# Optimization experiments

Measured on AMD Instinct MI355X. Metric: run time of the kernel, lower is better.

The kernel has to match this reference:

```python
import jax, jax.numpy as jnp
import numpy as np

B, H, S, D = 4, 16, 2048, 64

def setup_inputs() -> dict:
    key = jax.random.key(0)
    kq, kk, kv = jax.random.split(key, 3)
    Q = jax.random.normal(kq, (B, H, S, D), dtype=jnp.float32)
    K = jax.random.normal(kk, (B, H, S, D), dtype=jnp.float32)
    V = jax.random.normal(kv, (B, H, S, D), dtype=jnp.float32)
    return {"Q": Q, "K": K, "V": V}

def reference(Q, K, V):
    d_model = Q.shape[-1]
    # [B,H,S,S] scores matrix, materialized as in the original (unfused SDPA)
    scores = jnp.einsum('bhqd,bhkd->bhqk', Q, K) / jnp.sqrt(jnp.float32(d_model))
    attention = jax.nn.softmax(scores, axis=-1)
    out = jnp.einsum('bhqk,bhkd->bhqd', attention, V)
    return out
```

## Files before the change

kernel.cpp:

```cpp
#include <hip/hip_runtime.h>
#include <hip/hip_bf16.h>

namespace {

constexpr int kSeq = 2048;
constexpr int kD   = 64;
constexpr int kBH  = 64;
constexpr int kBM  = 64;
constexpr int kBN  = 64;
constexpr int kNT  = kSeq / kBN;
constexpr int kPs  = 72;

typedef __attribute__((ext_vector_type(8))) short bf16x8;
typedef __attribute__((ext_vector_type(4))) float f32x4;
typedef __attribute__((ext_vector_type(2))) unsigned int u32x2;

__device__ __forceinline__ unsigned short f2bf(float f) {
  unsigned int u = __builtin_bit_cast(unsigned int, f);
  u += 0x7fffu + ((u >> 16) & 1u);
  return (unsigned short)(u >> 16);
}

__device__ __forceinline__ unsigned int pkbf(float a, float b) {
#if __has_builtin(__builtin_amdgcn_cvt_pk_bf16_f32)
  typedef __attribute__((ext_vector_type(2))) __bf16 bfv2;
  bfv2 r = __builtin_amdgcn_cvt_pk_bf16_f32(a, b);
  return __builtin_bit_cast(unsigned int, r);
#else
  unsigned int ua = __builtin_bit_cast(unsigned int, a) + 0x8000u;
  unsigned int ub = __builtin_bit_cast(unsigned int, b) + 0x8000u;
  return __builtin_amdgcn_perm(ub, ua, 0x07060302);
#endif
}

__device__ __forceinline__ float fexp2(float x) {
#if __has_builtin(__builtin_amdgcn_exp2f)
  return __builtin_amdgcn_exp2f(x);
#else
  return exp2f(x);
#endif
}

__device__ __forceinline__ void load16(const unsigned short* g, unsigned short* l) {
  __builtin_amdgcn_global_load_lds(
      (const __attribute__((address_space(1))) unsigned int*)g,
      (__attribute__((address_space(3))) unsigned int*)l, 16, 0, 0);
}

__global__ __launch_bounds__(256) void prep(
    const float* __restrict__ K, const float* __restrict__ V,
    unsigned short* __restrict__ Kbf, unsigned short* __restrict__ Vt) {
  __shared__ unsigned short sT[kD * 72];
  const int tid = threadIdx.x;
  const int bh = blockIdx.x >> 5;
  const int t0 = (blockIdx.x & 31) * 64;
  const float* Kb = K + ((size_t)bh * kSeq + t0) * kD;
  const float* Vb = V + ((size_t)bh * kSeq + t0) * kD;
  unsigned short* Ko = Kbf + ((size_t)bh * kSeq + t0) * kD;
#pragma unroll
  for (int t = 0; t < 4; ++t) {
    const int idx = tid + t * 256;
    const int row = idx >> 4;
    const int c4  = (idx & 15) * 4;
    const float4 k4 = *(const float4*)(Kb + row * kD + c4);
    u32x2 kp = {pkbf(k4.x, k4.y), pkbf(k4.z, k4.w)};
    *(u32x2*)(Ko + row * kD + c4) = kp;
    const float4 v4 = *(const float4*)(Vb + row * kD + c4);
    sT[(c4 + 0) * 72 + row] = f2bf(v4.x);
    sT[(c4 + 1) * 72 + row] = f2bf(v4.y);
    sT[(c4 + 2) * 72 + row] = f2bf(v4.z);
    sT[(c4 + 3) * 72 + row] = f2bf(v4.w);
  }
  __syncthreads();
  const int d = tid >> 2, q = tid & 3;
  unsigned short* vo = Vt + ((size_t)bh * kD + d) * kSeq + t0 + q * 16;
  const unsigned short* ts = &sT[d * 72 + q * 16];
  *(uint4*)(vo)     = *(const uint4*)(ts);
  *(uint4*)(vo + 8) = *(const uint4*)(ts + 8);
}

__global__ __launch_bounds__(256, 3) void fattn4(
    const float* __restrict__ Q, const unsigned short* __restrict__ Kbf,
    const unsigned short* __restrict__ Vt, float* __restrict__ O) {
  __shared__ unsigned short sK[2][kBN * kD];
  __shared__ unsigned short sV[2][kD * kBN];
  __shared__ unsigned short sP[4 * 16 * kD];

  const int tid  = threadIdx.x;
  const int wave = tid >> 6;
  const int lane = tid & 63;
  const int quad = lane >> 4;
  const int l16  = lane & 15;
  const int swz  = l16 & 7;

  const int bh = blockIdx.x >> 5;
  const int q0 = (blockIdx.x & 31) * kBM;
  const size_t kb = (size_t)bh * kSeq * kD;

  constexpr float cs = 0.18033688011112042f;

  bf16x8 qf[2];
  {
    const float* qr = Q + kb + (size_t)(q0 + wave * 16 + l16) * kD + quad * 8;
#pragma unroll
    for (int kc = 0; kc < 2; ++kc)
#pragma unroll
      for (int j = 0; j < 8; ++j)
        qf[kc][j] = (short)f2bf(qr[kc * 32 + j] * cs);
  }

  bf16x8 ones;
#pragma unroll
  for (int j = 0; j < 8; ++j) ones[j] = (short)0x3F80;

  const int i0 = wave * 128 + lane;
  const int i1 = i0 + 64;
  const int r0 = i0 >> 3, c0 = (i0 & 7) ^ (r0 & 7);
  const int r1 = i1 >> 3, c1 = (i1 & 7) ^ (r1 & 7);
  const unsigned short* kg0 = Kbf + kb + r0 * kD + c0 * 8;
  const unsigned short* kg1 = Kbf + kb + r1 * kD + c1 * 8;
  const unsigned short* vg0 = Vt + kb + r0 * kSeq + c0 * 8;
  const unsigned short* vg1 = Vt + kb + r1 * kSeq + c1 * 8;

  f32x4 o[4];
#pragma unroll
  for (int dt = 0; dt < 4; ++dt) o[dt] = (f32x4){0.f, 0.f, 0.f, 0.f};
  f32x4 lacc = (f32x4){0.f, 0.f, 0.f, 0.f};

  unsigned short* pw = &sP[(wave * 16 + l16) * kD];

  load16(kg0, &sK[0][(wave * 2 + 0) * 512]);
  load16(kg1, &sK[0][(wave * 2 + 1) * 512]);
  load16(vg0, &sV[0][(wave * 2 + 0) * 512]);
  load16(vg1, &sV[0][(wave * 2 + 1) * 512]);

  for (int t = 0; t < kNT; ++t) {
    const int p = t & 1;
    __syncthreads();
    if (t + 1 < kNT) {
      const int pn = p ^ 1;
      const size_t ko = (size_t)(t + 1) * kBN * kD;
      const int vo = (t + 1) * kBN;
      load16(kg0 + ko, &sK[pn][(wave * 2 + 0) * 512]);
      load16(kg1 + ko, &sK[pn][(wave * 2 + 1) * 512]);
      load16(vg0 + vo, &sV[pn][(wave * 2 + 0) * 512]);
      load16(vg1 + vo, &sV[pn][(wave * 2 + 1) * 512]);
    }
    const unsigned short* sKp = sK[p];
    const unsigned short* sVp = sV[p];

    f32x4 s[4];
#pragma unroll
    for (int nt = 0; nt < 4; ++nt) s[nt] = (f32x4){0.f, 0.f, 0.f, 0.f};
#pragma unroll
    for (int kc = 0; kc < 2; ++kc)
#pragma unroll
      for (int nt = 0; nt < 4; ++nt) {
        const bf16x8 kf = *(const bf16x8*)&sKp[(nt * 16 + l16) * kD +
                                              (((kc * 4 + quad) ^ swz) * 8)];
        s[nt] = __builtin_amdgcn_mfma_f32_16x16x32_bf16(kf, qf[kc], s[nt], 0, 0, 0);
      }

#pragma unroll
    for (int nt = 0; nt < 4; ++nt) {
      const float p0 = fexp2(s[nt][0]);
      const float p1 = fexp2(s[nt][1]);
      const float p2 = fexp2(s[nt][2]);
      const float p3 = fexp2(s[nt][3]);
      u32x2 pp = {pkbf(p0, p1), pkbf(p2, p3)};
      const int pc = ((nt * 2 + (quad >> 1)) ^ swz) * 8 + (quad & 1) * 4;
      *(u32x2*)&pw[pc] = pp;
    }

#pragma unroll
    for (int kc = 0; kc < 2; ++kc) {
      const bf16x8 af = *(const bf16x8*)&pw[((kc * 4 + quad) ^ swz) * 8];
#pragma unroll
      for (int dt = 0; dt < 4; ++dt) {
        const bf16x8 vf = *(const bf16x8*)&sVp[(dt * 16 + l16) * kBN +
                                               (((kc * 4 + quad) ^ swz) * 8)];
        o[dt] = __builtin_amdgcn_mfma_f32_16x16x32_bf16(af, vf, o[dt], 0, 0, 0);
      }
      lacc = __builtin_amdgcn_mfma_f32_16x16x32_bf16(af, ones, lacc, 0, 0, 0);
    }
  }

  float* Ob = O + kb + (size_t)(q0 + wave * 16) * kD;
#pragma unroll
  for (int r = 0; r < 4; ++r) {
    const float inv = 1.f / lacc[r];
#pragma unroll
    for (int dt = 0; dt < 4; ++dt)
      Ob[(quad * 4 + r) * kD + dt * 16 + l16] = o[dt][r] * inv;
  }
}

__global__ __launch_bounds__(256, 4) void fattn_fb(
    const float* __restrict__ Q, const float* __restrict__ K,
    const float* __restrict__ V, float* __restrict__ O) {
  __shared__ unsigned short sK[kBN * kPs];
  __shared__ unsigned short sV[kD * kPs];
  __shared__ unsigned short sP[4 * 16 * kPs];
  const int tid = threadIdx.x, wave = tid >> 6, lane = tid & 63;
  const int quad = lane >> 4, l16 = lane & 15;
  const int bh = blockIdx.x >> 5, q0 = (blockIdx.x & 31) * kBM;
  const float* Qb = Q + (size_t)bh * kSeq * kD;
  const float* Kb = K + (size_t)bh * kSeq * kD;
  const float* Vb = V + (size_t)bh * kSeq * kD;
  bf16x8 qf[2];
  {
    const float* qr = Qb + (size_t)(q0 + wave * 16 + l16) * kD + quad * 8;
#pragma unroll
    for (int kc = 0; kc < 2; ++kc)
#pragma unroll
      for (int j = 0; j < 8; ++j) qf[kc][j] = (short)f2bf(qr[kc * 32 + j]);
  }
  f32x4 o[4];
#pragma unroll
  for (int dt = 0; dt < 4; ++dt) o[dt] = (f32x4){0.f, 0.f, 0.f, 0.f};
  float lsum[4] = {0.f, 0.f, 0.f, 0.f};
  constexpr float cs = 0.18033688011112042f;
  unsigned short* pw = &sP[wave * 16 * kPs];
  for (int kv0 = 0; kv0 < kSeq; kv0 += kBN) {
    __syncthreads();
#pragma unroll
    for (int t = 0; t < 4; ++t) {
      const int idx = tid + t * 256;
      const int row = idx >> 4, c4 = (idx & 15) * 4;
      const float4 k4 = *(const float4*)(Kb + (size_t)(kv0 + row) * kD + c4);
      unsigned short* kd = &sK[row * kPs + c4];
      kd[0] = f2bf(k4.x); kd[1] = f2bf(k4.y); kd[2] = f2bf(k4.z); kd[3] = f2bf(k4.w);
      const float4 v4 = *(const float4*)(Vb + (size_t)(kv0 + row) * kD + c4);
      sV[(c4 + 0) * kPs + row] = f2bf(v4.x);
      sV[(c4 + 1) * kPs + row] = f2bf(v4.y);
      sV[(c4 + 2) * kPs + row] = f2bf(v4.z);
      sV[(c4 + 3) * kPs + row] = f2bf(v4.w);
    }
    __syncthreads();
    f32x4 s[4];
#pragma unroll
    for (int nt = 0; nt < 4; ++nt) s[nt] = (f32x4){0.f, 0.f, 0.f, 0.f};
#pragma unroll
    for (int kc = 0; kc < 2; ++kc)
#pragma unroll
      for (int nt = 0; nt < 4; ++nt) {
        const bf16x8 kf = *(const bf16x8*)&sK[(nt * 16 + l16) * kPs + kc * 32 + quad * 8];
        s[nt] = __builtin_amdgcn_mfma_f32_16x16x32_bf16(qf[kc], kf, s[nt], 0, 0, 0);
      }
#pragma unroll
    for (int nt = 0; nt < 4; ++nt)
#pragma unroll
      for (int r = 0; r < 4; ++r) {
        const float p = fexp2(s[nt][r] * cs);
        lsum[r] += p;
        pw[(quad * 4 + r) * kPs + nt * 16 + l16] = f2bf(p);
      }
#pragma unroll
    for (int kc = 0; kc < 2; ++kc) {
      const bf16x8 af = *(const bf16x8*)&pw[l16 * kPs + kc * 32 + quad * 8];
#pragma unroll
      for (int dt = 0; dt < 4; ++dt) {
        const bf16x8 vf = *(const bf16x8*)&sV[(dt * 16 + l16) * kPs + kc * 32 + quad * 8];
        o[dt] = __builtin_amdgcn_mfma_f32_16x16x32_bf16(af, vf, o[dt], 0, 0, 0);
      }
    }
  }
#pragma unroll
  for (int r = 0; r < 4; ++r)
#pragma unroll
    for (int off = 1; off < 16; off <<= 1)
      lsum[r] += __shfl_xor(lsum[r], off, 64);
  float* Ob = O + (size_t)bh * kSeq * kD + (size_t)(q0 + wave * 16) * kD;
#pragma unroll
  for (int r = 0; r < 4; ++r) {
    const float inv = 1.f / lsum[r];
#pragma unroll
    for (int dt = 0; dt < 4; ++dt)
      Ob[(quad * 4 + r) * kD + dt * 16 + l16] = o[dt][r] * inv;
  }
}

}

extern "C" void kernel_launch(void* const* d_in, const int* in_sizes, int n_in,
                              void* d_out, int out_size, void* d_ws, size_t ws_size,
                              hipStream_t stream) {
  const float* Q = (const float*)d_in[0];
  const float* K = (const float*)d_in[1];
  const float* V = (const float*)d_in[2];
  float* Oo = (float*)d_out;
  const size_t need = (size_t)2 * kBH * kSeq * kD * sizeof(unsigned short);
  if (ws_size >= need) {
    unsigned short* Kbf = (unsigned short*)d_ws;
    unsigned short* Vt  = Kbf + (size_t)kBH * kSeq * kD;
    prep<<<dim3(kBH * (kSeq / 64)), dim3(256), 0, stream>>>(K, V, Kbf, Vt);
    fattn4<<<dim3(kBH * (kSeq / kBM)), dim3(256), 0, stream>>>(Q, Kbf, Vt, Oo);
  } else {
    fattn_fb<<<dim3(kBH * (kSeq / kBM)), dim3(256), 0, stream>>>(Q, K, V, Oo);
  }
}
```

Before: 223.3 us.

## Use 128-query blocks with 8 waves sharing K/V tiles and remap block order

The flash-attention kernel now runs 512 threads (8 waves) per block over 128 query rows, so each K/V tile staged in LDS is reused by twice as many query rows and global traffic for K/V is halved. Block indices are remapped so consecutive blocks span different heads, which likely spreads work across XCDs and L2. The prep kernel transposes V through a padded fp32 LDS tile and packs to bf16 with vector conversions instead of scalar 16-bit stores. In exchange, larger blocks mean fewer blocks in the grid and higher LDS use per block, which could hurt occupancy and tail balance.

```diff
diff --git a/kernel.cpp b/kernel.cpp
--- a/kernel.cpp
+++ b/kernel.cpp
@@ -6,7 +6,7 @@
 constexpr int kSeq = 2048;
 constexpr int kD   = 64;
 constexpr int kBH  = 64;
-constexpr int kBM  = 64;
+constexpr int kQB  = 128;
 constexpr int kBN  = 64;
 constexpr int kNT  = kSeq / kBN;
 constexpr int kPs  = 72;
@@ -50,7 +50,7 @@
 __global__ __launch_bounds__(256) void prep(
     const float* __restrict__ K, const float* __restrict__ V,
     unsigned short* __restrict__ Kbf, unsigned short* __restrict__ Vt) {
-  __shared__ unsigned short sT[kD * 72];
+  __shared__ float sTf[kD * 65];
   const int tid = threadIdx.x;
   const int bh = blockIdx.x >> 5;
   const int t0 = (blockIdx.x & 31) * 64;
@@ -66,25 +66,33 @@
     u32x2 kp = {pkbf(k4.x, k4.y), pkbf(k4.z, k4.w)};
     *(u32x2*)(Ko + row * kD + c4) = kp;
     const float4 v4 = *(const float4*)(Vb + row * kD + c4);
-    sT[(c4 + 0) * 72 + row] = f2bf(v4.x);
-    sT[(c4 + 1) * 72 + row] = f2bf(v4.y);
-    sT[(c4 + 2) * 72 + row] = f2bf(v4.z);
-    sT[(c4 + 3) * 72 + row] = f2bf(v4.w);
+    sTf[(c4 + 0) * 65 + row] = v4.x;
+    sTf[(c4 + 1) * 65 + row] = v4.y;
+    sTf[(c4 + 2) * 65 + row] = v4.z;
+    sTf[(c4 + 3) * 65 + row] = v4.w;
   }
   __syncthreads();
   const int d = tid >> 2, q = tid & 3;
+  const float* ts = &sTf[d * 65 + q * 16];
+  float p[16];
+#pragma unroll
+  for (int j = 0; j < 16; ++j) p[j] = ts[j];
+  uint4 a, b;
+  a.x = pkbf(p[0], p[1]);   a.y = pkbf(p[2], p[3]);
+  a.z = pkbf(p[4], p[5]);   a.w = pkbf(p[6], p[7]);
+  b.x = pkbf(p[8], p[9]);   b.y = pkbf(p[10], p[11]);
+  b.z = pkbf(p[12], p[13]); b.w = pkbf(p[14], p[15]);
   unsigned short* vo = Vt + ((size_t)bh * kD + d) * kSeq + t0 + q * 16;
-  const unsigned short* ts = &sT[d * 72 + q * 16];
-  *(uint4*)(vo)     = *(const uint4*)(ts);
-  *(uint4*)(vo + 8) = *(const uint4*)(ts + 8);
-}
-
-__global__ __launch_bounds__(256, 3) void fattn4(
+  *(uint4*)(vo)     = a;
+  *(uint4*)(vo + 8) = b;
+}
+
+__global__ __launch_bounds__(512, 6) void fattn5(
     const float* __restrict__ Q, const unsigned short* __restrict__ Kbf,
     const unsigned short* __restrict__ Vt, float* __restrict__ O) {
   __shared__ unsigned short sK[2][kBN * kD];
   __shared__ unsigned short sV[2][kD * kBN];
-  __shared__ unsigned short sP[4 * 16 * kD];
+  __shared__ unsigned short sP[8 * 16 * kD];
 
   const int tid  = threadIdx.x;
   const int wave = tid >> 6;
@@ -93,8 +101,10 @@
   const int l16  = lane & 15;
   const int swz  = l16 & 7;
 
-  const int bh = blockIdx.x >> 5;
-  const int q0 = (blockIdx.x & 31) * kBM;
+  const int x  = blockIdx.x & 7;
+  const int j  = blockIdx.x >> 3;
+  const int bh = x * 8 + (j >> 4);
+  const int q0 = (j & 15) * kQB;
   const size_t kb = (size_t)bh * kSeq * kD;
 
   constexpr float cs = 0.18033688011112042f;
@@ -105,22 +115,17 @@
 #pragma unroll
     for (int kc = 0; kc < 2; ++kc)
 #pragma unroll
-      for (int j = 0; j < 8; ++j)
-        qf[kc][j] = (short)f2bf(qr[kc * 32 + j] * cs);
+      for (int jj = 0; jj < 8; ++jj)
+        qf[kc][jj] = (short)f2bf(qr[kc * 32 + jj] * cs);
   }
 
   bf16x8 ones;
 #pragma unroll
-  for (int j = 0; j < 8; ++j) ones[j] = (short)0x3F80;
-
-  const int i0 = wave * 128 + lane;
-  const int i1 = i0 + 64;
-  const int r0 = i0 >> 3, c0 = (i0 & 7) ^ (r0 & 7);
-  const int r1 = i1 >> 3, c1 = (i1 & 7) ^ (r1 & 7);
+  for (int jj = 0; jj < 8; ++jj) ones[jj] = (short)0x3F80;
+
+  const int r0 = tid >> 3, c0 = (tid & 7) ^ (r0 & 7);
   const unsigned short* kg0 = Kbf + kb + r0 * kD + c0 * 8;
-  const unsigned short* kg1 = Kbf + kb + r1 * kD + c1 * 8;
   const unsigned short* vg0 = Vt + kb + r0 * kSeq + c0 * 8;
-  const unsigned short* vg1 = Vt + kb + r1 * kSeq + c1 * 8;
 
   f32x4 o[4];
 #pragma unroll
@@ -129,22 +134,16 @@
 
   unsigned short* pw = &sP[(wave * 16 + l16) * kD];
 
-  load16(kg0, &sK[0][(wave * 2 + 0) * 512]);
-  load16(kg1, &sK[0][(wave * 2 + 1) * 512]);
-  load16(vg0, &sV[0][(wave * 2 + 0) * 512]);
-  load16(vg1, &sV[0][(wave * 2 + 1) * 512]);
+  load16(kg0, &sK[0][wave * 512]);
+  load16(vg0, &sV[0][wave * 512]);
 
   for (int t = 0; t < kNT; ++t) {
     const int p = t & 1;
     __syncthreads();
     if (t + 1 < kNT) {
       const int pn = p ^ 1;
-      const size_t ko = (size_t)(t + 1) * kBN * kD;
-      const int vo = (t + 1) * kBN;
-      load16(kg0 + ko, &sK[pn][(wave * 2 + 0) * 512]);
-      load16(kg1 + ko, &sK[pn][(wave * 2 + 1) * 512]);
-      load16(vg0 + vo, &sV[pn][(wave * 2 + 0) * 512]);
-      load16(vg1 + vo, &sV[pn][(wave * 2 + 1) * 512]);
+      load16(kg0 + (size_t)(t + 1) * kBN * kD, &sK[pn][wave * 512]);
+      load16(vg0 + (t + 1) * kBN, &sV[pn][wave * 512]);
     }
     const unsigned short* sKp = sK[p];
     const unsigned short* sVp = sV[p];
@@ -203,7 +202,7 @@
   __shared__ unsigned short sP[4 * 16 * kPs];
   const int tid = threadIdx.x, wave = tid >> 6, lane = tid & 63;
   const int quad = lane >> 4, l16 = lane & 15;
-  const int bh = blockIdx.x >> 5, q0 = (blockIdx.x & 31) * kBM;
+  const int bh = blockIdx.x >> 5, q0 = (blockIdx.x & 31) * 64;
   const float* Qb = Q + (size_t)bh * kSeq * kD;
   const float* Kb = K + (size_t)bh * kSeq * kD;
   const float* Vb = V + (size_t)bh * kSeq * kD;
@@ -213,7 +212,7 @@
 #pragma unroll
     for (int kc = 0; kc < 2; ++kc)
 #pragma unroll
-      for (int j = 0; j < 8; ++j) qf[kc][j] = (short)f2bf(qr[kc * 32 + j]);
+      for (int jj = 0; jj < 8; ++jj) qf[kc][jj] = (short)f2bf(qr[kc * 32 + jj]);
   }
   f32x4 o[4];
 #pragma unroll
@@ -294,8 +293,8 @@
     unsigned short* Kbf = (unsigned short*)d_ws;
     unsigned short* Vt  = Kbf + (size_t)kBH * kSeq * kD;
     prep<<<dim3(kBH * (kSeq / 64)), dim3(256), 0, stream>>>(K, V, Kbf, Vt);
-    fattn4<<<dim3(kBH * (kSeq / kBM)), dim3(256), 0, stream>>>(Q, Kbf, Vt, Oo);
+    fattn5<<<dim3(kBH * (kSeq / kQB)), dim3(512), 0, stream>>>(Q, Kbf, Vt, Oo);
   } else {
-    fattn_fb<<<dim3(kBH * (kSeq / kBM)), dim3(256), 0, stream>>>(Q, K, V, Oo);
-  }
-}
+    fattn_fb<<<dim3(kBH * (kSeq / 64)), dim3(256), 0, stream>>>(Q, K, V, Oo);
+  }
+}
```

Measured after the change: 213.8 us. 4.3% less time.
